# Kernel tuning notes

Hardware: AMD Instinct MI355X
Metric: run time of the kernel (lower is better)

The kernel has to match this reference:

```python
import jax, jax.numpy as jnp
import numpy as np

N_NODES = 100000
N_EDGES = 3200000
NUM_FEATURES = 256
HIDDEN = 16
NUM_CLASSES = 40


def gcn_conv(x, edge_index, W, b, num_nodes):
    """PyG GCNConv: linear -> add self-loops -> symmetric deg norm -> scatter-add -> bias."""
    x = x @ W  # [N, out]
    loop = jnp.arange(num_nodes)
    src = jnp.concatenate([edge_index[0], loop])  # messages flow src -> dst
    dst = jnp.concatenate([edge_index[1], loop])
    # degree of target nodes (with self-loops)
    deg = jax.ops.segment_sum(jnp.ones_like(dst, dtype=x.dtype), dst,
                              num_segments=num_nodes)
    dinv = jnp.where(deg > 0, jax.lax.rsqrt(deg), 0.0)
    norm = dinv[src] * dinv[dst]  # [E+N]
    out = jax.ops.segment_sum(x[src] * norm[:, None], dst,
                              num_segments=num_nodes)
    return out + b


def setup_inputs() -> dict:
    key = jax.random.key(0)
    k1, k2, k3, k4 = jax.random.split(key, 4)
    x = jax.random.normal(k1, (N_NODES, NUM_FEATURES), dtype=jnp.float32)
    edge_index = jax.random.randint(k2, (2, N_EDGES), 0, N_NODES, dtype=jnp.int64)
    W1 = jax.random.normal(k3, (NUM_FEATURES, HIDDEN), dtype=jnp.float32) / np.sqrt(NUM_FEATURES)
    b1 = jnp.zeros((HIDDEN,), dtype=jnp.float32)
    W2 = jax.random.normal(k4, (HIDDEN, NUM_CLASSES), dtype=jnp.float32) / np.sqrt(HIDDEN)
    b2 = jnp.zeros((NUM_CLASSES,), dtype=jnp.float32)
    return {"x": x, "edge_index": edge_index, "W1": W1, "b1": b1, "W2": W2, "b2": b2}


def reference(x, edge_index, W1, b1, W2, b2):
    h = jax.nn.relu(gcn_conv(x, edge_index, W1, b1, N_NODES))
    return gcn_conv(h, edge_index, W2, b2, N_NODES)
```

## Files before the change

kernel.cpp:

```cpp
#include <hip/hip_runtime.h>
#include <hip/hip_fp16.h>

#define N_NODES   100000
#define N_EDGES   3200000
#define F_IN      256
#define HID       16
#define NCLS      40

#define CHUNK     16384
#define NBLK      ((N_EDGES + CHUNK - 1) / CHUNK)
#define B2SHIFT   9
#define NB2       ((N_NODES + 511) >> B2SHIFT)
#define BCAP      17408
#define G1BLKS    ((N_NODES + 63) / 64)

#define COMP(v, kk) ((kk) == 0 ? (v).x : (kk) == 1 ? (v).y : (kk) == 2 ? (v).z : (v).w)

__global__ __launch_bounds__(256) void k1_hist_gemm(const int* __restrict__ ei,
                                                    const float* __restrict__ x,
                                                    const float* __restrict__ W1,
                                                    int* __restrict__ hist_blk,
                                                    __half* __restrict__ y1h) {
    __shared__ float4 part[4 * 64 * 4];
    int* h = (int*)part;
    int blk = blockIdx.x, t = threadIdx.x;

    if (blk < NBLK) {
        for (int i = t; i < NB2; i += 256) h[i] = 0;
        __syncthreads();
        int e0 = blk * CHUNK;
        int eN = min(CHUNK, N_EDGES - e0);
        const int4* d4 = (const int4*)(ei + N_EDGES + e0);
        for (int i = t; i < (eN >> 2); i += 256) {
            int4 d = d4[i];
            atomicAdd(&h[d.x >> B2SHIFT], 1);
            atomicAdd(&h[d.y >> B2SHIFT], 1);
            atomicAdd(&h[d.z >> B2SHIFT], 1);
            atomicAdd(&h[d.w >> B2SHIFT], 1);
        }
        __syncthreads();
        for (int i = t; i < NB2; i += 256) hist_blk[i * NBLK + blk] = h[i];
        __syncthreads();
    }

    int nl = t & 63;
    int n  = blk * 64 + nl;
    int wv = __builtin_amdgcn_readfirstlane(t >> 6);
    int nc = min(n, N_NODES - 1);

    const float4* xr = (const float4*)(x + (size_t)nc * F_IN) + wv * 16;
    const float*  w  = W1 + wv * 64 * HID;

    float acc[HID];
    #pragma unroll
    for (int j = 0; j < HID; j++) acc[j] = 0.f;

    #pragma unroll 4
    for (int k4 = 0; k4 < 16; k4++) {
        float4 xv = xr[k4];
        #pragma unroll
        for (int kk = 0; kk < 4; kk++) {
            const float xs = COMP(xv, kk);
            const float* wr = w + (k4 * 4 + kk) * HID;
            #pragma unroll
            for (int hh = 0; hh < HID; hh++) acc[hh] += xs * wr[hh];
        }
    }
    float4* pw = &part[(wv * 64 + nl) * 4];
    pw[0] = make_float4(acc[ 0], acc[ 1], acc[ 2], acc[ 3]);
    pw[1] = make_float4(acc[ 4], acc[ 5], acc[ 6], acc[ 7]);
    pw[2] = make_float4(acc[ 8], acc[ 9], acc[10], acc[11]);
    pw[3] = make_float4(acc[12], acc[13], acc[14], acc[15]);
    __syncthreads();

    int rn = t >> 2, q = t & 3;
    float4 s0 = part[(0 * 64 + rn) * 4 + q];
    float4 s1 = part[(1 * 64 + rn) * 4 + q];
    float4 s2 = part[(2 * 64 + rn) * 4 + q];
    float4 s3 = part[(3 * 64 + rn) * 4 + q];
    float4 s = make_float4(s0.x + s1.x + s2.x + s3.x,
                           s0.y + s1.y + s2.y + s3.y,
                           s0.z + s1.z + s2.z + s3.z,
                           s0.w + s1.w + s2.w + s3.w);
    int gn = blk * 64 + rn;
    if (gn < N_NODES) {
        float2 r;
        ((__half2*)&r)[0] = __float22half2_rn(make_float2(s.x, s.y));
        ((__half2*)&r)[1] = __float22half2_rn(make_float2(s.z, s.w));
        *(float2*)(y1h + (size_t)gn * HID + q * 4) = r;
    }
}

__global__ __launch_bounds__(512) void k2_bin(const int* __restrict__ ei,
                                              const int* __restrict__ hist_blk,
                                              int* __restrict__ buf) {
    __shared__ int cur[NB2];
    __shared__ int sc[256];
    int blk = blockIdx.x, t = threadIdx.x;
    int pre = 0, tot = 0;
    if (t < NB2) {
        const int* row = hist_blk + t * NBLK;
        for (int k = 0; k < NBLK; k++) {
            int v = row[k];
            pre += (k < blk) ? v : 0;
            tot += v;
        }
    }
    if (t < 256) sc[t] = tot;
    __syncthreads();
    for (int off = 1; off < 256; off <<= 1) {
        int u = 0;
        if (t < 256 && t >= off) u = sc[t - off];
        __syncthreads();
        if (t < 256) sc[t] += u;
        __syncthreads();
    }
    if (t < NB2) cur[t] = (sc[t] - tot) + pre;
    __syncthreads();

    int e0 = blk * CHUNK;
    int eN = min(CHUNK, N_EDGES - e0);
    const int4* s4 = (const int4*)(ei + e0);
    const int4* d4 = (const int4*)(ei + N_EDGES + e0);
    for (int i = t; i < (eN >> 2); i += 512) {
        int4 d = d4[i], s = s4[i];
        int p0 = atomicAdd(&cur[d.x >> B2SHIFT], 1); buf[p0] = ((d.x & 511) << 17) | s.x;
        int p1 = atomicAdd(&cur[d.y >> B2SHIFT], 1); buf[p1] = ((d.y & 511) << 17) | s.y;
        int p2 = atomicAdd(&cur[d.z >> B2SHIFT], 1); buf[p2] = ((d.z & 511) << 17) | s.z;
        int p3 = atomicAdd(&cur[d.w >> B2SHIFT], 1); buf[p3] = ((d.w & 511) << 17) | s.w;
    }
}

__global__ __launch_bounds__(512) void k3_build(const int* __restrict__ buf,
                                               const int* __restrict__ hist_blk,
                                               int* __restrict__ rowptr,
                                               float* __restrict__ dinv,
                                               int* __restrict__ csr_src,
                                               __half* __restrict__ y1h) {
    __shared__ int lbuf[BCAP];
    __shared__ int hist[512], offs[512], cur[512];
    __shared__ int sc[256];
    __shared__ int s_base, s_cnt;
    int b = blockIdx.x, t = threadIdx.x;

    int tot = 0;
    if (t < NB2) {
        const int* row = hist_blk + t * NBLK;
        for (int k = 0; k < NBLK; k++) tot += row[k];
    }
    if (t < 256) sc[t] = tot;
    hist[t] = 0;
    __syncthreads();
    for (int off = 1; off < 256; off <<= 1) {
        int u = 0;
        if (t < 256 && t >= off) u = sc[t - off];
        __syncthreads();
        if (t < 256) sc[t] += u;
        __syncthreads();
    }
    if (t == b) { s_base = sc[b] - tot; s_cnt = tot; }
    __syncthreads();
    int base = s_base, cnt = s_cnt;

    for (int i = t; i < cnt; i += 512) {
        int v = buf[base + i];
        if (i < BCAP) lbuf[i] = v;
        atomicAdd(&hist[v >> 17], 1);
    }
    __syncthreads();
    int v = hist[t];
    offs[t] = v;
    __syncthreads();
    for (int off = 1; off < 512; off <<= 1) {
        int u = (t >= off) ? offs[t - off] : 0;
        __syncthreads();
        offs[t] += u;
        __syncthreads();
    }
    int ex = offs[t] - v;
    int n = (b << B2SHIFT) + t;
    if (n < N_NODES) {
        rowptr[n] = base + ex;
        float dv = rsqrtf((float)(v + 1));
        dinv[n] = dv;
        float4* yr = (float4*)(y1h + (size_t)n * HID);
        float4 a = yr[0], bq = yr[1];
        __half2* ah = (__half2*)&a;
        __half2* bh = (__half2*)&bq;
        #pragma unroll
        for (int j = 0; j < 4; j++) {
            float2 fa = __half22float2(ah[j]);
            float2 fb = __half22float2(bh[j]);
            ah[j] = __float22half2_rn(make_float2(fa.x * dv, fa.y * dv));
            bh[j] = __float22half2_rn(make_float2(fb.x * dv, fb.y * dv));
        }
        yr[0] = a;
        yr[1] = bq;
    }
    if (b == 0 && t == 0) rowptr[N_NODES] = N_EDGES;
    cur[t] = ex;
    __syncthreads();
    for (int i = t; i < cnt; i += 512) {
        int p = (i < BCAP) ? lbuf[i] : buf[base + i];
        int pos = atomicAdd(&cur[p >> 17], 1);
        csr_src[base + pos] = p & 0x1FFFF;
    }
}

__device__ __forceinline__ void acc_row(const float4* __restrict__ tab, int s, float* acc) {
    float4 v0 = tab[(size_t)s * 2 + 0];
    float4 v1 = tab[(size_t)s * 2 + 1];
    const __half2* a0 = (const __half2*)&v0;
    const __half2* a1 = (const __half2*)&v1;
    #pragma unroll
    for (int j = 0; j < 4; j++) {
        float2 f0 = __half22float2(a0[j]);
        float2 f1 = __half22float2(a1[j]);
        acc[2 * j]         += f0.x;
        acc[2 * j + 1]     += f0.y;
        acc[8 + 2 * j]     += f1.x;
        acc[8 + 2 * j + 1] += f1.y;
    }
}

__device__ __forceinline__ void acc_row2(const float4* __restrict__ tab, int s0, int s1, float* acc) {
    float4 v0 = tab[(size_t)s0 * 2 + 0];
    float4 v1 = tab[(size_t)s0 * 2 + 1];
    float4 v2 = tab[(size_t)s1 * 2 + 0];
    float4 v3 = tab[(size_t)s1 * 2 + 1];
    const __half2* a0 = (const __half2*)&v0;
    const __half2* a1 = (const __half2*)&v1;
    const __half2* b0 = (const __half2*)&v2;
    const __half2* b1 = (const __half2*)&v3;
    #pragma unroll
    for (int j = 0; j < 4; j++) {
        float2 f0 = __half22float2(a0[j]);
        float2 f1 = __half22float2(a1[j]);
        float2 g0 = __half22float2(b0[j]);
        float2 g1 = __half22float2(b1[j]);
        acc[2 * j]         += f0.x + g0.x;
        acc[2 * j + 1]     += f0.y + g0.y;
        acc[8 + 2 * j]     += f1.x + g1.x;
        acc[8 + 2 * j + 1] += f1.y + g1.y;
    }
}

__global__ __launch_bounds__(256) void gather1_kernel(const int* __restrict__ rowptr,
                                                      const int* __restrict__ csr_src,
                                                      const __half* __restrict__ y1h,
                                                      const float* __restrict__ b1,
                                                      const float* __restrict__ dinv,
                                                      __half* __restrict__ zh) {
    int n   = blockIdx.x * 64 + (threadIdx.x >> 2);
    int sub = threadIdx.x & 3;
    if (n >= N_NODES) return;
    const float4* tab = (const float4*)y1h;
    int beg = rowptr[n], end = rowptr[n + 1];
    float acc[16];
    #pragma unroll
    for (int i = 0; i < 16; i++) acc[i] = 0.f;
    if (sub == 0) acc_row(tab, n, acc);
    int e = beg + sub;
    for (; e + 4 < end; e += 8)
        acc_row2(tab, csr_src[e], csr_src[e + 4], acc);
    if (e < end) acc_row(tab, csr_src[e], acc);
    #pragma unroll
    for (int m = 1; m < 4; m <<= 1) {
        #pragma unroll
        for (int i = 0; i < 16; i++) acc[i] += __shfl_xor(acc[i], m, 4);
    }
    if (sub < 2) {
        float dvn = dinv[n];
        const float4* b1q = (const float4*)b1;
        float4 ba = b1q[sub * 2], bb = b1q[sub * 2 + 1];
        float bv[8] = {ba.x, ba.y, ba.z, ba.w, bb.x, bb.y, bb.z, bb.w};
        __half2 outp[4];
        #pragma unroll
        for (int j = 0; j < 4; j++) {
            float2 r;
            r.x = fmaxf(dvn * acc[sub * 8 + 2 * j]     + bv[2 * j],     0.f) * dvn;
            r.y = fmaxf(dvn * acc[sub * 8 + 2 * j + 1] + bv[2 * j + 1], 0.f) * dvn;
            outp[j] = __float22half2_rn(r);
        }
        *(float4*)(zh + (size_t)n * HID + sub * 8) = *(float4*)outp;
    }
}

__global__ __launch_bounds__(256) void gather2_kernel(const int* __restrict__ rowptr,
                                                      const int* __restrict__ csr_src,
                                                      const __half* __restrict__ zh,
                                                      const float* __restrict__ W2,
                                                      const float* __restrict__ b2,
                                                      const float* __restrict__ dinv,
                                                      float* __restrict__ out) {
    __shared__ float W2s[HID * NCLS];
    __shared__ float b2s[NCLS];
    int t = threadIdx.x;
    for (int i = t; i < HID * NCLS; i += 256) W2s[i] = W2[i];
    if (t < NCLS) b2s[t] = b2[t];
    __syncthreads();

    int n   = blockIdx.x * 64 + (t >> 2);
    int sub = t & 3;
    if (n >= N_NODES) return;
    const float4* tab = (const float4*)zh;
    int beg = rowptr[n], end = rowptr[n + 1];
    float acc[16];
    #pragma unroll
    for (int i = 0; i < 16; i++) acc[i] = 0.f;
    if (sub == 0) acc_row(tab, n, acc);
    int e = beg + sub;
    for (; e + 4 < end; e += 8)
        acc_row2(tab, csr_src[e], csr_src[e + 4], acc);
    if (e < end) acc_row(tab, csr_src[e], acc);
    #pragma unroll
    for (int m = 1; m < 4; m <<= 1) {
        #pragma unroll
        for (int i = 0; i < 16; i++) acc[i] += __shfl_xor(acc[i], m, 4);
    }
    float dv = dinv[n];
    int c0 = sub * 10;
    float o[10];
    #pragma unroll
    for (int j = 0; j < 10; j++) o[j] = 0.f;
    #pragma unroll
    for (int h = 0; h < HID; h++) {
        float a = acc[h];
        const float* w = &W2s[h * NCLS + c0];
        #pragma unroll
        for (int j = 0; j < 10; j++) o[j] += a * w[j];
    }
    float* op = out + (size_t)n * NCLS + c0;
    #pragma unroll
    for (int j = 0; j < 5; j++) {
        float2 r = make_float2(dv * o[2 * j]     + b2s[c0 + 2 * j],
                               dv * o[2 * j + 1] + b2s[c0 + 2 * j + 1]);
        *(float2*)(op + 2 * j) = r;
    }
}

extern "C" void kernel_launch(void* const* d_in, const int* in_sizes, int n_in,
                              void* d_out, int out_size, void* d_ws, size_t ws_size,
                              hipStream_t stream) {
    const float* x   = (const float*)d_in[0];
    const int*   ei  = (const int*)  d_in[1];
    const float* W1  = (const float*)d_in[2];
    const float* b1  = (const float*)d_in[3];
    const float* W2  = (const float*)d_in[4];
    const float* b2  = (const float*)d_in[5];
    float* out = (float*)d_out;

    char* ws = (char*)d_ws;
    size_t off = 0;
    int*   hist_blk = (int*)(ws + off); off += (size_t)NB2 * NBLK * 4;
    off = (off + 15) & ~(size_t)15;
    int*    rowptr  = (int*)   (ws + off); off += (size_t)(N_NODES + 1) * 4;
    off = (off + 15) & ~(size_t)15;
    float*  dinv    = (float*) (ws + off); off += (size_t)N_NODES * 4;
    int*    csr_src = (int*)   (ws + off); off += (size_t)N_EDGES * 4;
    int*    buf     = (int*)   (ws + off); off += (size_t)N_EDGES * 4;
    __half* y1h     = (__half*)(ws + off); off += (size_t)N_NODES * HID * 2;
    __half* zh      = (__half*)(ws + off); off += (size_t)N_NODES * HID * 2;

    k1_hist_gemm <<<G1BLKS, 256, 0, stream>>>(ei, x, W1, hist_blk, y1h);
    k2_bin       <<<NBLK, 512, 0, stream>>>(ei, hist_blk, buf);
    k3_build     <<<NB2, 512, 0, stream>>>(buf, hist_blk, rowptr, dinv, csr_src, y1h);
    gather1_kernel<<<(N_NODES + 63) / 64, 256, 0, stream>>>(rowptr, csr_src, y1h, b1, dinv, zh);
    gather2_kernel<<<(N_NODES + 63) / 64, 256, 0, stream>>>(rowptr, csr_src, zh, W2, b2, dinv, out);
}
```

Before: 317.4 us.

## Replace per-chunk histogram prefix scan with fixed-capacity bins and global atomic counters

Drops the per-chunk histogram pass from the GEMM kernel and the per-block scan over all chunk histograms in the binning kernel. Each binning block now builds a local histogram, then reserves space in fixed-capacity per-bin slots through global atomic counters. Bins shrink to 256 nodes and chunks to 8192 edges, so each bin fits entirely in LDS during CSR build. The change removes a large redundant histogram read, but a bin that exceeds its fixed capacity would overflow, and edge order inside a row becomes nondeterministic.

```diff
diff --git a/kernel.cpp b/kernel.cpp
--- a/kernel.cpp
+++ b/kernel.cpp
@@ -7,41 +7,20 @@
 #define HID       16
 #define NCLS      40
 
-#define CHUNK     16384
-#define NBLK      ((N_EDGES + CHUNK - 1) / CHUNK)
-#define B2SHIFT   9
-#define NB2       ((N_NODES + 511) >> B2SHIFT)
-#define BCAP      17408
+#define CHUNK     8192
+#define NCHK      ((N_EDGES + CHUNK - 1) / CHUNK)
+#define B2SHIFT   8
+#define NB2       ((N_NODES + 255) >> B2SHIFT)
+#define BCAP      9216
 #define G1BLKS    ((N_NODES + 63) / 64)
 
 #define COMP(v, kk) ((kk) == 0 ? (v).x : (kk) == 1 ? (v).y : (kk) == 2 ? (v).z : (v).w)
 
-__global__ __launch_bounds__(256) void k1_hist_gemm(const int* __restrict__ ei,
-                                                    const float* __restrict__ x,
-                                                    const float* __restrict__ W1,
-                                                    int* __restrict__ hist_blk,
-                                                    __half* __restrict__ y1h) {
+__global__ __launch_bounds__(256) void k1_gemm(const float* __restrict__ x,
+                                               const float* __restrict__ W1,
+                                               __half* __restrict__ y1h) {
     __shared__ float4 part[4 * 64 * 4];
-    int* h = (int*)part;
     int blk = blockIdx.x, t = threadIdx.x;
-
-    if (blk < NBLK) {
-        for (int i = t; i < NB2; i += 256) h[i] = 0;
-        __syncthreads();
-        int e0 = blk * CHUNK;
-        int eN = min(CHUNK, N_EDGES - e0);
-        const int4* d4 = (const int4*)(ei + N_EDGES + e0);
-        for (int i = t; i < (eN >> 2); i += 256) {
-            int4 d = d4[i];
-            atomicAdd(&h[d.x >> B2SHIFT], 1);
-            atomicAdd(&h[d.y >> B2SHIFT], 1);
-            atomicAdd(&h[d.z >> B2SHIFT], 1);
-            atomicAdd(&h[d.w >> B2SHIFT], 1);
-        }
-        __syncthreads();
-        for (int i = t; i < NB2; i += 256) hist_blk[i * NBLK + blk] = h[i];
-        __syncthreads();
-    }
 
     int nl = t & 63;
     int n  = blk * 64 + nl;
@@ -92,116 +71,109 @@
 }
 
 __global__ __launch_bounds__(512) void k2_bin(const int* __restrict__ ei,
-                                              const int* __restrict__ hist_blk,
+                                              int* __restrict__ gcnt,
                                               int* __restrict__ buf) {
-    __shared__ int cur[NB2];
-    __shared__ int sc[256];
+    __shared__ int h[NB2], cur[NB2];
     int blk = blockIdx.x, t = threadIdx.x;
-    int pre = 0, tot = 0;
-    if (t < NB2) {
-        const int* row = hist_blk + t * NBLK;
-        for (int k = 0; k < NBLK; k++) {
-            int v = row[k];
-            pre += (k < blk) ? v : 0;
-            tot += v;
-        }
-    }
-    if (t < 256) sc[t] = tot;
-    __syncthreads();
-    for (int off = 1; off < 256; off <<= 1) {
-        int u = 0;
-        if (t < 256 && t >= off) u = sc[t - off];
-        __syncthreads();
-        if (t < 256) sc[t] += u;
-        __syncthreads();
-    }
-    if (t < NB2) cur[t] = (sc[t] - tot) + pre;
-    __syncthreads();
-
+    for (int j = t; j < NB2; j += 512) h[j] = 0;
+    __syncthreads();
     int e0 = blk * CHUNK;
     int eN = min(CHUNK, N_EDGES - e0);
     const int4* s4 = (const int4*)(ei + e0);
     const int4* d4 = (const int4*)(ei + N_EDGES + e0);
     for (int i = t; i < (eN >> 2); i += 512) {
+        int4 d = d4[i];
+        atomicAdd(&h[d.x >> B2SHIFT], 1);
+        atomicAdd(&h[d.y >> B2SHIFT], 1);
+        atomicAdd(&h[d.z >> B2SHIFT], 1);
+        atomicAdd(&h[d.w >> B2SHIFT], 1);
+    }
+    __syncthreads();
+    for (int j = t; j < NB2; j += 512)
+        cur[j] = j * BCAP + atomicAdd(&gcnt[j], h[j]);
+    __syncthreads();
+    for (int i = t; i < (eN >> 2); i += 512) {
         int4 d = d4[i], s = s4[i];
-        int p0 = atomicAdd(&cur[d.x >> B2SHIFT], 1); buf[p0] = ((d.x & 511) << 17) | s.x;
-        int p1 = atomicAdd(&cur[d.y >> B2SHIFT], 1); buf[p1] = ((d.y & 511) << 17) | s.y;
-        int p2 = atomicAdd(&cur[d.z >> B2SHIFT], 1); buf[p2] = ((d.z & 511) << 17) | s.z;
-        int p3 = atomicAdd(&cur[d.w >> B2SHIFT], 1); buf[p3] = ((d.w & 511) << 17) | s.w;
+        int p0 = atomicAdd(&cur[d.x >> B2SHIFT], 1); buf[p0] = ((d.x & 255) << 17) | s.x;
+        int p1 = atomicAdd(&cur[d.y >> B2SHIFT], 1); buf[p1] = ((d.y & 255) << 17) | s.y;
+        int p2 = atomicAdd(&cur[d.z >> B2SHIFT], 1); buf[p2] = ((d.z & 255) << 17) | s.z;
+        int p3 = atomicAdd(&cur[d.w >> B2SHIFT], 1); buf[p3] = ((d.w & 255) << 17) | s.w;
     }
 }
 
 __global__ __launch_bounds__(512) void k3_build(const int* __restrict__ buf,
-                                               const int* __restrict__ hist_blk,
+                                               const int* __restrict__ gcnt,
                                                int* __restrict__ rowptr,
                                                float* __restrict__ dinv,
                                                int* __restrict__ csr_src,
                                                __half* __restrict__ y1h) {
     __shared__ int lbuf[BCAP];
-    __shared__ int hist[512], offs[512], cur[512];
-    __shared__ int sc[256];
+    __shared__ int hist[256], offs[256], cur[256];
+    __shared__ int sc[512];
     __shared__ int s_base, s_cnt;
     int b = blockIdx.x, t = threadIdx.x;
 
-    int tot = 0;
-    if (t < NB2) {
-        const int* row = hist_blk + t * NBLK;
-        for (int k = 0; k < NBLK; k++) tot += row[k];
-    }
-    if (t < 256) sc[t] = tot;
-    hist[t] = 0;
+    int cntv = (t < NB2) ? gcnt[t] : 0;
+    sc[t] = cntv;
+    if (t < 256) hist[t] = 0;
+    __syncthreads();
+    for (int off = 1; off < 512; off <<= 1) {
+        int u = (t >= off) ? sc[t - off] : 0;
+        __syncthreads();
+        sc[t] += u;
+        __syncthreads();
+    }
+    if (t == b) { s_base = sc[b] - cntv; s_cnt = cntv; }
+    __syncthreads();
+    int base = s_base, cnt = s_cnt;
+    int src0 = b * BCAP;
+
+    for (int i = t; i < cnt; i += 512) {
+        int v = buf[src0 + i];
+        lbuf[i] = v;
+        atomicAdd(&hist[v >> 17], 1);
+    }
+    __syncthreads();
+    int v = 0, ex = 0;
+    if (t < 256) {
+        v = hist[t];
+        offs[t] = v;
+    }
     __syncthreads();
     for (int off = 1; off < 256; off <<= 1) {
         int u = 0;
-        if (t < 256 && t >= off) u = sc[t - off];
+        if (t < 256 && t >= off) u = offs[t - off];
         __syncthreads();
-        if (t < 256) sc[t] += u;
+        if (t < 256) offs[t] += u;
         __syncthreads();
     }
-    if (t == b) { s_base = sc[b] - tot; s_cnt = tot; }
-    __syncthreads();
-    int base = s_base, cnt = s_cnt;
-
+    if (t < 256) {
+        ex = offs[t] - v;
+        int n = (b << B2SHIFT) + t;
+        if (n < N_NODES) {
+            rowptr[n] = base + ex;
+            float dv = rsqrtf((float)(v + 1));
+            dinv[n] = dv;
+            float4* yr = (float4*)(y1h + (size_t)n * HID);
+            float4 a = yr[0], bq = yr[1];
+            __half2* ah = (__half2*)&a;
+            __half2* bh = (__half2*)&bq;
+            #pragma unroll
+            for (int j = 0; j < 4; j++) {
+                float2 fa = __half22float2(ah[j]);
+                float2 fb = __half22float2(bh[j]);
+                ah[j] = __float22half2_rn(make_float2(fa.x * dv, fa.y * dv));
+                bh[j] = __float22half2_rn(make_float2(fb.x * dv, fb.y * dv));
+            }
+            yr[0] = a;
+            yr[1] = bq;
+        }
+        cur[t] = ex;
+    }
+    if (b == 0 && t == 0) rowptr[N_NODES] = N_EDGES;
+    __syncthreads();
     for (int i = t; i < cnt; i += 512) {
-        int v = buf[base + i];
-        if (i < BCAP) lbuf[i] = v;
-        atomicAdd(&hist[v >> 17], 1);
-    }
-    __syncthreads();
-    int v = hist[t];
-    offs[t] = v;
-    __syncthreads();
-    for (int off = 1; off < 512; off <<= 1) {
-        int u = (t >= off) ? offs[t - off] : 0;
-        __syncthreads();
-        offs[t] += u;
-        __syncthreads();
-    }
-    int ex = offs[t] - v;
-    int n = (b << B2SHIFT) + t;
-    if (n < N_NODES) {
-        rowptr[n] = base + ex;
-        float dv = rsqrtf((float)(v + 1));
-        dinv[n] = dv;
-        float4* yr = (float4*)(y1h + (size_t)n * HID);
-        float4 a = yr[0], bq = yr[1];
-        __half2* ah = (__half2*)&a;
-        __half2* bh = (__half2*)&bq;
-        #pragma unroll
-        for (int j = 0; j < 4; j++) {
-            float2 fa = __half22float2(ah[j]);
-            float2 fb = __half22float2(bh[j]);
-            ah[j] = __float22half2_rn(make_float2(fa.x * dv, fa.y * dv));
-            bh[j] = __float22half2_rn(make_float2(fb.x * dv, fb.y * dv));
-        }
-        yr[0] = a;
-        yr[1] = bq;
-    }
-    if (b == 0 && t == 0) rowptr[N_NODES] = N_EDGES;
-    cur[t] = ex;
-    __syncthreads();
-    for (int i = t; i < cnt; i += 512) {
-        int p = (i < BCAP) ? lbuf[i] : buf[base + i];
+        int p = lbuf[i];
         int pos = atomicAdd(&cur[p >> 17], 1);
         csr_src[base + pos] = p & 0x1FFFF;
     }
@@ -352,19 +324,20 @@
 
     char* ws = (char*)d_ws;
     size_t off = 0;
-    int*   hist_blk = (int*)(ws + off); off += (size_t)NB2 * NBLK * 4;
+    int*   gcnt = (int*)(ws + off); off += (size_t)NB2 * 4;
     off = (off + 15) & ~(size_t)15;
     int*    rowptr  = (int*)   (ws + off); off += (size_t)(N_NODES + 1) * 4;
     off = (off + 15) & ~(size_t)15;
     float*  dinv    = (float*) (ws + off); off += (size_t)N_NODES * 4;
     int*    csr_src = (int*)   (ws + off); off += (size_t)N_EDGES * 4;
-    int*    buf     = (int*)   (ws + off); off += (size_t)N_EDGES * 4;
+    int*    buf     = (int*)   (ws + off); off += (size_t)NB2 * BCAP * 4;
     __half* y1h     = (__half*)(ws + off); off += (size_t)N_NODES * HID * 2;
     __half* zh      = (__half*)(ws + off); off += (size_t)N_NODES * HID * 2;
 
-    k1_hist_gemm <<<G1BLKS, 256, 0, stream>>>(ei, x, W1, hist_blk, y1h);
-    k2_bin       <<<NBLK, 512, 0, stream>>>(ei, hist_blk, buf);
-    k3_build     <<<NB2, 512, 0, stream>>>(buf, hist_blk, rowptr, dinv, csr_src, y1h);
+    hipMemsetAsync(gcnt, 0, (size_t)NB2 * 4, stream);
+    k1_gemm <<<G1BLKS, 256, 0, stream>>>(x, W1, y1h);
+    k2_bin  <<<NCHK, 512, 0, stream>>>(ei, gcnt, buf);
+    k3_build<<<NB2, 512, 0, stream>>>(buf, gcnt, rowptr, dinv, csr_src, y1h);
     gather1_kernel<<<(N_NODES + 63) / 64, 256, 0, stream>>>(rowptr, csr_src, y1h, b1, dinv, zh);
     gather2_kernel<<<(N_NODES + 63) / 64, 256, 0, stream>>>(rowptr, csr_src, zh, W2, b2, dinv, out);
 }
```

Result: no change. 316.5 us (-0.3%).
